# Optimization experiments

Hardware: AMD Instinct MI355X
Metric: run time of the kernel (lower is better)

The kernel has to match this reference:

```python
import jax, jax.numpy as jnp
import numpy as np

N_NODES = 100000
N_EDGES = 1600000
IN_FEATS = 128
HIDDEN = 128
NUM_CLASSES = 4


def setup_inputs() -> dict:
    key = jax.random.key(0)
    ks = jax.random.split(key, 8)
    features = jax.random.normal(ks[0], (N_NODES, IN_FEATS), dtype=jnp.float32)
    src = jax.random.randint(ks[1], (N_EDGES,), 0, N_NODES, dtype=jnp.int64)
    dst = jax.random.randint(ks[2], (N_EDGES,), 0, N_NODES, dtype=jnp.int64)
    s = 1.0 / np.sqrt(IN_FEATS)
    W1 = jax.random.normal(ks[3], (IN_FEATS, HIDDEN), dtype=jnp.float32) * s
    b1 = jnp.zeros((HIDDEN,), dtype=jnp.float32)
    W2 = jax.random.normal(ks[4], (HIDDEN, HIDDEN), dtype=jnp.float32) * s
    b2 = jnp.zeros((HIDDEN,), dtype=jnp.float32)
    Wc = jax.random.normal(ks[5], (HIDDEN, NUM_CLASSES), dtype=jnp.float32) * s
    bc = jnp.zeros((NUM_CLASSES,), dtype=jnp.float32)
    return {"features": features, "src": src, "dst": dst,
            "W1": W1, "b1": b1, "W2": W2, "b2": b2, "Wc": Wc, "bc": bc}


def _graph_conv(x, W, b, src, dst, n_nodes, activation=True):
    # DGL GraphConv, norm='both': D_out^{-1/2} A^T D_in... i.e. symmetric norm.
    ones = jnp.ones((src.shape[0],), dtype=x.dtype)
    deg_out = jnp.clip(jax.ops.segment_sum(ones, src, num_segments=n_nodes), 1.0)
    deg_in = jnp.clip(jax.ops.segment_sum(ones, dst, num_segments=n_nodes), 1.0)
    # scale sources, project (in >= out so matmul first, math-equivalent), gather-scatter
    h = (x * (deg_out ** -0.5)[:, None]) @ W            # [N, out]
    msg = h[src]                                         # [E, out] gather
    agg = jax.ops.segment_sum(msg, dst, num_segments=n_nodes)  # [N, out] scatter-add
    h = agg * (deg_in ** -0.5)[:, None] + b
    return jax.nn.relu(h) if activation else h


def reference(features, src, dst, W1, b1, W2, b2, Wc, bc):
    # eval-mode forward: dropout is identity
    n = features.shape[0]
    h = _graph_conv(features, W1, b1, src, dst, n, activation=True)
    h = _graph_conv(h, W2, b2, src, dst, n, activation=True)
    return h @ Wc + bc  # [N, num_classes] logits
```

## Files before the change

kernel.cpp:

```cpp
#include <hip/hip_runtime.h>
#include <hip/hip_fp16.h>
#include <math.h>

#define N_NODES 100000
#define N_EDGES 1600000
#define F 128
#define NBUK 196
#define BSH 9
#define BSZ 512
#define CAP 10240
#define NPART 784

typedef _Float16 half8 __attribute__((ext_vector_type(8)));
typedef float    f32x4 __attribute__((ext_vector_type(4)));
typedef int      i32x4 __attribute__((ext_vector_type(4)));

__global__ __launch_bounds__(256) void init_pack(int* __restrict__ curD,
                                                 int* __restrict__ curS,
                                                 _Float16* __restrict__ padrow1,
                                                 _Float16* __restrict__ padrow2,
                                                 const float* __restrict__ W1,
                                                 const float* __restrict__ W2,
                                                 _Float16* __restrict__ hi1,
                                                 _Float16* __restrict__ lo1,
                                                 _Float16* __restrict__ hi2,
                                                 _Float16* __restrict__ lo2)
{
    int t = threadIdx.x;
    if (blockIdx.x == 0) {
        if (t < NBUK) { curD[t] = t * CAP; curS[t] = t * CAP; }
        if (t < 16) reinterpret_cast<int4*>(padrow1)[t] = make_int4(0, 0, 0, 0);
        else if (t >= 32 && t < 48) reinterpret_cast<int4*>(padrow2)[t - 32] = make_int4(0, 0, 0, 0);
        return;
    }
    int gidx = (blockIdx.x - 1) * 256 + t;
    const float* W = (gidx < 16384) ? W1 : W2;
    _Float16* hi = (gidx < 16384) ? hi1 : hi2;
    _Float16* lo = (gidx < 16384) ? lo1 : lo2;
    int idx = gidx & 16383;
    int f = idx >> 9, r = idx & 511;
    int l = r >> 3, j = r & 7;
    int kc = f >> 3, ct = f & 7;
    int k = kc * 32 + (l >> 4) * 8 + j;
    int n = ct * 16 + (l & 15);
    float w = W[k * 128 + n];
    _Float16 h = (_Float16)w;
    hi[idx] = h;
    lo[idx] = (_Float16)(w - (float)h);
}

__global__ __launch_bounds__(512) void part_edges(const int* __restrict__ src,
                                                  const int* __restrict__ dst,
                                                  int* __restrict__ curD,
                                                  int* __restrict__ curS,
                                                  int* __restrict__ bukD,
                                                  unsigned short* __restrict__ bukS)
{
    __shared__ int hd[NBUK], hs[NBUK], bd[NBUK], bs[NBUK], cd[NBUK], cs[NBUK];
    const int tid = threadIdx.x;
    const int chunk = (((N_EDGES + NPART - 1) / NPART) + 3) & ~3;
    const int beg = blockIdx.x * chunk;
    const int end = min(beg + chunk, N_EDGES);
    if (beg >= end) return;
    if (tid < NBUK) { hd[tid] = 0; hs[tid] = 0; cd[tid] = 0; cs[tid] = 0; }
    __syncthreads();
    const int b4 = beg >> 2, e4 = end >> 2;
    const int i0 = b4 + tid;
    const bool v0 = i0 < e4;
    i32x4 d0 = {}, s0 = {};
    if (v0) {
        d0 = reinterpret_cast<const i32x4*>(dst)[i0];
        s0 = reinterpret_cast<const i32x4*>(src)[i0];
        atomicAdd(&hd[d0.x >> BSH], 1); atomicAdd(&hd[d0.y >> BSH], 1);
        atomicAdd(&hd[d0.z >> BSH], 1); atomicAdd(&hd[d0.w >> BSH], 1);
        atomicAdd(&hs[s0.x >> BSH], 1); atomicAdd(&hs[s0.y >> BSH], 1);
        atomicAdd(&hs[s0.z >> BSH], 1); atomicAdd(&hs[s0.w >> BSH], 1);
    }
    __syncthreads();
    if (tid < NBUK) {
        bd[tid] = hd[tid] ? atomicAdd(&curD[tid], hd[tid]) : 0;
        bs[tid] = hs[tid] ? atomicAdd(&curS[tid], hs[tid]) : 0;
    }
    __syncthreads();
    if (v0) {
        int dd[4] = { d0.x, d0.y, d0.z, d0.w };
        int ss[4] = { s0.x, s0.y, s0.z, s0.w };
        #pragma unroll
        for (int j = 0; j < 4; j++) {
            int bin = dd[j] >> BSH;
            int r = atomicAdd(&cd[bin], 1);
            bukD[bd[bin] + r] = ((dd[j] & 511) << 17) | ss[j];
            int bin2 = ss[j] >> BSH;
            int r2 = atomicAdd(&cs[bin2], 1);
            bukS[bs[bin2] + r2] = (unsigned short)(ss[j] & 511);
        }
    }
}

__global__ __launch_bounds__(512) void deg_out(const unsigned short* __restrict__ bukS,
                                               const int* __restrict__ curS,
                                               float* __restrict__ sout)
{
    __shared__ int h[BSZ];
    const int tid = threadIdx.x;
    const int n0 = blockIdx.x << BSH;
    const int lo = blockIdx.x * CAP, hi = curS[blockIdx.x];
    const int cnt = hi - lo;
    h[tid] = 0;
    __syncthreads();
    const uint4* p8 = reinterpret_cast<const uint4*>(bukS + lo);
    const int nv = cnt >> 3;
    for (int j = tid; j < nv; j += 512) {
        uint4 v = p8[j];
        atomicAdd(&h[v.x & 0xFFFF], 1); atomicAdd(&h[v.x >> 16], 1);
        atomicAdd(&h[v.y & 0xFFFF], 1); atomicAdd(&h[v.y >> 16], 1);
        atomicAdd(&h[v.z & 0xFFFF], 1); atomicAdd(&h[v.z >> 16], 1);
        atomicAdd(&h[v.w & 0xFFFF], 1); atomicAdd(&h[v.w >> 16], 1);
    }
    for (int i = lo + (nv << 3) + tid; i < hi; i += 512)
        atomicAdd(&h[bukS[i]], 1);
    __syncthreads();
    int node = n0 + tid;
    if (node < N_NODES) sout[node] = rsqrtf((float)max(h[tid], 1));
}

__global__ __launch_bounds__(512) void csr_gemm1(const int* __restrict__ bukD,
                                                 const int* __restrict__ curD,
                                                 int* __restrict__ row_ptr,
                                                 float* __restrict__ sin_,
                                                 int* __restrict__ col,
                                                 const float* __restrict__ X,
                                                 const _Float16* __restrict__ Whi,
                                                 const _Float16* __restrict__ Wlo,
                                                 const float* __restrict__ sout,
                                                 _Float16* __restrict__ Y, int N)
{
    __shared__ int h[BSZ], sc[BSZ], cur[BSZ];
    const int tid = threadIdx.x;

    if (blockIdx.x < NBUK) {
        const int n0 = blockIdx.x << BSH;
        const int lo = blockIdx.x * CAP, hi = curD[blockIdx.x];
        const int cnt = hi - lo;
        h[tid] = 0;
        __syncthreads();
        const i32x4* p4 = reinterpret_cast<const i32x4*>(bukD + lo);
        const int nv = cnt >> 2;
        for (int j = tid; j < nv; j += 512) {
            i32x4 v = p4[j];
            atomicAdd(&h[((unsigned)v.x) >> 17], 1);
            atomicAdd(&h[((unsigned)v.y) >> 17], 1);
            atomicAdd(&h[((unsigned)v.z) >> 17], 1);
            atomicAdd(&h[((unsigned)v.w) >> 17], 1);
        }
        for (int i = lo + (nv << 2) + tid; i < hi; i += 512)
            atomicAdd(&h[((unsigned)bukD[i]) >> 17], 1);
        __syncthreads();
        int own = h[tid];
        int own4 = (own + 3) & ~3;
        sc[tid] = own4;
        __syncthreads();
        for (int off = 1; off < 512; off <<= 1) {
            int u = (tid >= off) ? sc[tid - off] : 0;
            __syncthreads();
            sc[tid] += u;
            __syncthreads();
        }
        int ex = sc[tid] - own4;
        cur[tid] = ex;
        int node = n0 + tid;
        if (node < N_NODES) {
            row_ptr[2 * node]     = lo + ex;
            row_ptr[2 * node + 1] = lo + ex + own4;
            sin_[node] = rsqrtf((float)max(own, 1));
        }
        __syncthreads();
        for (int j = tid; j < nv; j += 512) {
            i32x4 v = p4[j];
            int pv[4] = { v.x, v.y, v.z, v.w };
            #pragma unroll
            for (int q = 0; q < 4; q++) {
                int p = pv[q];
                int r = atomicAdd(&cur[((unsigned)p) >> 17], 1);
                col[lo + r] = p & 0x1FFFF;
            }
        }
        for (int i = lo + (nv << 2) + tid; i < hi; i += 512) {
            int p = bukD[i];
            int r = atomicAdd(&cur[((unsigned)p) >> 17], 1);
            col[lo + r] = p & 0x1FFFF;
        }
        for (int k = own; k < own4; k++)
            col[lo + ex + k] = N_NODES;
        return;
    }

    const int l = tid & 63, w = tid >> 6;
    const int quad = l >> 4, m = l & 15;
    const int row0 = (blockIdx.x - NBUK) * 256;
    const half8* Bh = reinterpret_cast<const half8*>(Whi);
    const half8* Bl = reinterpret_cast<const half8*>(Wlo);

    f32x4 acc[2][8] = {};

    for (int kc = 0; kc < 4; kc++) {
        half8 ah[2];
        #pragma unroll
        for (int rt = 0; rt < 2; rt++) {
            int grow = row0 + w * 32 + rt * 16 + m;
            float4 xa = make_float4(0.f, 0.f, 0.f, 0.f), xb = xa;
            if (grow < N) {
                const float4* Xp = reinterpret_cast<const float4*>(X) + (size_t)grow * 32 + kc * 8 + quad * 2;
                xa = Xp[0]; xb = Xp[1];
            }
            ah[rt][0] = (_Float16)xa.x; ah[rt][1] = (_Float16)xa.y;
            ah[rt][2] = (_Float16)xa.z; ah[rt][3] = (_Float16)xa.w;
            ah[rt][4] = (_Float16)xb.x; ah[rt][5] = (_Float16)xb.y;
            ah[rt][6] = (_Float16)xb.z; ah[rt][7] = (_Float16)xb.w;
        }
        #pragma unroll
        for (int ct = 0; ct < 8; ct++) {
            int f = kc * 8 + ct;
            half8 bh = Bh[f * 64 + l];
            half8 bl = Bl[f * 64 + l];
            #pragma unroll
            for (int rt = 0; rt < 2; rt++) {
                acc[rt][ct] = __builtin_amdgcn_mfma_f32_16x16x32_f16(ah[rt], bh, acc[rt][ct], 0, 0, 0);
                acc[rt][ct] = __builtin_amdgcn_mfma_f32_16x16x32_f16(ah[rt], bl, acc[rt][ct], 0, 0, 0);
            }
        }
    }

    #pragma unroll
    for (int rt = 0; rt < 2; rt++) {
        #pragma unroll
        for (int r = 0; r < 4; r++) {
            int grow = row0 + w * 32 + rt * 16 + quad * 4 + r;
            if (grow < N) {
                float s = sout[grow];
                #pragma unroll
                for (int ct = 0; ct < 8; ct++)
                    Y[(size_t)grow * 128 + ct * 16 + m] = (_Float16)(acc[rt][ct][r] * s);
            }
        }
    }
}

#define ACCU(vv) \
    a0 += (float)vv[0]; a1 += (float)vv[1]; a2 += (float)vv[2]; a3 += (float)vv[3]; \
    a4 += (float)vv[4]; a5 += (float)vv[5]; a6 += (float)vv[6]; a7 += (float)vv[7];

__global__ __launch_bounds__(256) void gather_gemm2(const _Float16* __restrict__ Hh,
                                                    const int* __restrict__ row_ptr,
                                                    const int* __restrict__ col,
                                                    const float* __restrict__ sin_,
                                                    const float* __restrict__ bias,
                                                    const _Float16* __restrict__ Whi,
                                                    const _Float16* __restrict__ Wlo,
                                                    const float* __restrict__ sout,
                                                    _Float16* __restrict__ Y)
{
    __shared__ _Float16 At[16][128];
    const int tid = threadIdx.x;
    const int sub  = tid & 15;
    const int g0   = tid >> 4;
    const int node = blockIdx.x * 16 + g0;
    const int beg = row_ptr[2 * node], end = row_ptr[2 * node + 1];
    const half8* __restrict__ H8 = reinterpret_cast<const half8*>(Hh);

    float a0 = 0.f, a1 = 0.f, a2 = 0.f, a3 = 0.f, a4 = 0.f, a5 = 0.f, a6 = 0.f, a7 = 0.f;
    int i = beg;
    for (; i + 8 <= end; i += 8) {
        int4 ca = *reinterpret_cast<const int4*>(col + i);
        int4 cb = *reinterpret_cast<const int4*>(col + i + 4);
        half8 v0 = H8[((size_t)ca.x << 4) | sub];
        half8 v1 = H8[((size_t)ca.y << 4) | sub];
        half8 v2 = H8[((size_t)ca.z << 4) | sub];
        half8 v3 = H8[((size_t)ca.w << 4) | sub];
        half8 v4 = H8[((size_t)cb.x << 4) | sub];
        half8 v5 = H8[((size_t)cb.y << 4) | sub];
        half8 v6 = H8[((size_t)cb.z << 4) | sub];
        half8 v7 = H8[((size_t)cb.w << 4) | sub];
        ACCU(v0) ACCU(v1) ACCU(v2) ACCU(v3)
        ACCU(v4) ACCU(v5) ACCU(v6) ACCU(v7)
    }
    if (i < end) {
        int4 ca = *reinterpret_cast<const int4*>(col + i);
        half8 v0 = H8[((size_t)ca.x << 4) | sub];
        half8 v1 = H8[((size_t)ca.y << 4) | sub];
        half8 v2 = H8[((size_t)ca.z << 4) | sub];
        half8 v3 = H8[((size_t)ca.w << 4) | sub];
        ACCU(v0) ACCU(v1) ACCU(v2) ACCU(v3)
    }
    {
        float scn = sin_[node];
        const float4* B4 = reinterpret_cast<const float4*>(bias);
        float4 bA = B4[2 * sub], bB = B4[2 * sub + 1];
        half8 o;
        o[0] = (_Float16)fmaxf(fmaf(a0, scn, bA.x), 0.f);
        o[1] = (_Float16)fmaxf(fmaf(a1, scn, bA.y), 0.f);
        o[2] = (_Float16)fmaxf(fmaf(a2, scn, bA.z), 0.f);
        o[3] = (_Float16)fmaxf(fmaf(a3, scn, bA.w), 0.f);
        o[4] = (_Float16)fmaxf(fmaf(a4, scn, bB.x), 0.f);
        o[5] = (_Float16)fmaxf(fmaf(a5, scn, bB.y), 0.f);
        o[6] = (_Float16)fmaxf(fmaf(a6, scn, bB.z), 0.f);
        o[7] = (_Float16)fmaxf(fmaf(a7, scn, bB.w), 0.f);
        int wc = sub ^ (g0 & 7);
        *reinterpret_cast<half8*>(&At[g0][wc * 8]) = o;
    }
    __syncthreads();

    const int l = tid & 63, w = tid >> 6;
    const int quad = l >> 4, m = l & 15;
    const half8* Bh = reinterpret_cast<const half8*>(Whi);
    const half8* Bl = reinterpret_cast<const half8*>(Wlo);

    f32x4 acc0 = {}, acc1 = {};
    #pragma unroll
    for (int kc = 0; kc < 4; kc++) {
        int rc = (kc * 4 + quad) ^ (m & 7);
        half8 a = *reinterpret_cast<const half8*>(&At[m][rc * 8]);
        int f0 = kc * 8 + w * 2;
        half8 bh0 = Bh[f0 * 64 + l];
        half8 bl0 = Bl[f0 * 64 + l];
        half8 bh1 = Bh[(f0 + 1) * 64 + l];
        half8 bl1 = Bl[(f0 + 1) * 64 + l];
        acc0 = __builtin_amdgcn_mfma_f32_16x16x32_f16(a, bh0, acc0, 0, 0, 0);
        acc0 = __builtin_amdgcn_mfma_f32_16x16x32_f16(a, bl0, acc0, 0, 0, 0);
        acc1 = __builtin_amdgcn_mfma_f32_16x16x32_f16(a, bh1, acc1, 0, 0, 0);
        acc1 = __builtin_amdgcn_mfma_f32_16x16x32_f16(a, bl1, acc1, 0, 0, 0);
    }

    const int rbase = blockIdx.x * 16 + quad * 4;
    const int c0 = (w * 2) * 16 + m;
    #pragma unroll
    for (int r = 0; r < 4; r++) {
        int grow = rbase + r;
        float s = sout[grow];
        Y[(size_t)grow * 128 + c0]      = (_Float16)(acc0[r] * s);
        Y[(size_t)grow * 128 + c0 + 16] = (_Float16)(acc1[r] * s);
    }
}

__global__ __launch_bounds__(256) void gather_cls(const _Float16* __restrict__ Hh,
                                                  const int* __restrict__ row_ptr,
                                                  const int* __restrict__ col,
                                                  const float* __restrict__ sin_,
                                                  const float* __restrict__ bias,
                                                  const float* __restrict__ Wc,
                                                  const float* __restrict__ bc,
                                                  float* __restrict__ out, int N)
{
    __shared__ float4 Wcs[128];
    for (int t = threadIdx.x; t < 128; t += 256)
        Wcs[t] = reinterpret_cast<const float4*>(Wc)[t];
    __syncthreads();

    const int sub  = threadIdx.x & 15;
    const int node = blockIdx.x * 16 + (threadIdx.x >> 4);
    if (node >= N) return;
    const int beg = row_ptr[2 * node], end = row_ptr[2 * node + 1];
    const half8* __restrict__ H8 = reinterpret_cast<const half8*>(Hh);

    float a0 = 0.f, a1 = 0.f, a2 = 0.f, a3 = 0.f, a4 = 0.f, a5 = 0.f, a6 = 0.f, a7 = 0.f;
    int i = beg;
    for (; i + 8 <= end; i += 8) {
        int4 ca = *reinterpret_cast<const int4*>(col + i);
        int4 cb = *reinterpret_cast<const int4*>(col + i + 4);
        half8 v0 = H8[((size_t)ca.x << 4) | sub];
        half8 v1 = H8[((size_t)ca.y << 4) | sub];
        half8 v2 = H8[((size_t)ca.z << 4) | sub];
        half8 v3 = H8[((size_t)ca.w << 4) | sub];
        half8 v4 = H8[((size_t)cb.x << 4) | sub];
        half8 v5 = H8[((size_t)cb.y << 4) | sub];
        half8 v6 = H8[((size_t)cb.z << 4) | sub];
        half8 v7 = H8[((size_t)cb.w << 4) | sub];
        ACCU(v0) ACCU(v1) ACCU(v2) ACCU(v3)
        ACCU(v4) ACCU(v5) ACCU(v6) ACCU(v7)
    }
    if (i < end) {
        int4 ca = *reinterpret_cast<const int4*>(col + i);
        half8 v0 = H8[((size_t)ca.x << 4) | sub];
        half8 v1 = H8[((size_t)ca.y << 4) | sub];
        half8 v2 = H8[((size_t)ca.z << 4) | sub];
        half8 v3 = H8[((size_t)ca.w << 4) | sub];
        ACCU(v0) ACCU(v1) ACCU(v2) ACCU(v3)
    }
    float scn = sin_[node];
    const float4* B4 = reinterpret_cast<const float4*>(bias);
    float4 bA = B4[2 * sub], bB = B4[2 * sub + 1];
    float h0 = fmaxf(fmaf(a0, scn, bA.x), 0.f);
    float h1 = fmaxf(fmaf(a1, scn, bA.y), 0.f);
    float h2 = fmaxf(fmaf(a2, scn, bA.z), 0.f);
    float h3 = fmaxf(fmaf(a3, scn, bA.w), 0.f);
    float h4 = fmaxf(fmaf(a4, scn, bB.x), 0.f);
    float h5 = fmaxf(fmaf(a5, scn, bB.y), 0.f);
    float h6 = fmaxf(fmaf(a6, scn, bB.z), 0.f);
    float h7 = fmaxf(fmaf(a7, scn, bB.w), 0.f);

    float lx = 0.f, ly = 0.f, lz = 0.f, lw = 0.f;
    float4 w;
    w = Wcs[sub * 8 + 0]; lx = fmaf(h0, w.x, lx); ly = fmaf(h0, w.y, ly); lz = fmaf(h0, w.z, lz); lw = fmaf(h0, w.w, lw);
    w = Wcs[sub * 8 + 1]; lx = fmaf(h1, w.x, lx); ly = fmaf(h1, w.y, ly); lz = fmaf(h1, w.z, lz); lw = fmaf(h1, w.w, lw);
    w = Wcs[sub * 8 + 2]; lx = fmaf(h2, w.x, lx); ly = fmaf(h2, w.y, ly); lz = fmaf(h2, w.z, lz); lw = fmaf(h2, w.w, lw);
    w = Wcs[sub * 8 + 3]; lx = fmaf(h3, w.x, lx); ly = fmaf(h3, w.y, ly); lz = fmaf(h3, w.z, lz); lw = fmaf(h3, w.w, lw);
    w = Wcs[sub * 8 + 4]; lx = fmaf(h4, w.x, lx); ly = fmaf(h4, w.y, ly); lz = fmaf(h4, w.z, lz); lw = fmaf(h4, w.w, lw);
    w = Wcs[sub * 8 + 5]; lx = fmaf(h5, w.x, lx); ly = fmaf(h5, w.y, ly); lz = fmaf(h5, w.z, lz); lw = fmaf(h5, w.w, lw);
    w = Wcs[sub * 8 + 6]; lx = fmaf(h6, w.x, lx); ly = fmaf(h6, w.y, ly); lz = fmaf(h6, w.z, lz); lw = fmaf(h6, w.w, lw);
    w = Wcs[sub * 8 + 7]; lx = fmaf(h7, w.x, lx); ly = fmaf(h7, w.y, ly); lz = fmaf(h7, w.z, lz); lw = fmaf(h7, w.w, lw);

    #pragma unroll
    for (int m = 1; m < 16; m <<= 1) {
        lx += __shfl_xor(lx, m);
        ly += __shfl_xor(ly, m);
        lz += __shfl_xor(lz, m);
        lw += __shfl_xor(lw, m);
    }
    if (sub == 0) {
        float4 bcv = reinterpret_cast<const float4*>(bc)[0];
        float4 r;
        r.x = lx + bcv.x; r.y = ly + bcv.y; r.z = lz + bcv.z; r.w = lw + bcv.w;
        reinterpret_cast<float4*>(out)[node] = r;
    }
}

extern "C" void kernel_launch(void* const* d_in, const int* in_sizes, int n_in,
                              void* d_out, int out_size, void* d_ws, size_t ws_size,
                              hipStream_t stream)
{
    const float* features = (const float*)d_in[0];
    const int*   src      = (const int*)d_in[1];
    const int*   dst      = (const int*)d_in[2];
    const float* W1       = (const float*)d_in[3];
    const float* b1       = (const float*)d_in[4];
    const float* W2       = (const float*)d_in[5];
    const float* b2       = (const float*)d_in[6];
    const float* Wc       = (const float*)d_in[7];
    const float* bc       = (const float*)d_in[8];
    float* out = (float*)d_out;

    char* ws = (char*)d_ws;
    const size_t MB = 1 << 20;
    int* curD  = (int*)(ws + 0);
    int* curS  = (int*)(ws + 1024);
    _Float16* Whi1 = (_Float16*)(ws + 64 * 1024);
    _Float16* Wlo1 = (_Float16*)(ws + 96 * 1024);
    _Float16* Whi2 = (_Float16*)(ws + 128 * 1024);
    _Float16* Wlo2 = (_Float16*)(ws + 160 * 1024);
    float* sout    = (float*)(ws + 512 * 1024);
    float* sin_    = (float*)(ws + 1 * MB);
    int*   row_ptr = (int*)(ws + 2 * MB);
    int*   col     = (int*)(ws + 3 * MB);
    _Float16* hMsg = (_Float16*)(ws + 25 * MB);
    int*   bukD    = (int*)(ws + 52 * MB);
    unsigned short* bukS = (unsigned short*)(ws + 60 * MB);
    _Float16* hA   = (_Float16*)(ws + 52 * MB);

    const int N = N_NODES;
    const int NGB = (N + 15) / 16;

    init_pack<<<129, 256, 0, stream>>>(curD, curS,
                                       hMsg + (size_t)N * F, hA + (size_t)N * F,
                                       W1, W2, Whi1, Wlo1, Whi2, Wlo2);

    part_edges<<<NPART, 512, 0, stream>>>(src, dst, curD, curS, bukD, bukS);

    deg_out<<<NBUK, 512, 0, stream>>>(bukS, curS, sout);

    csr_gemm1<<<NBUK + 391, 512, 0, stream>>>(bukD, curD, row_ptr, sin_, col,
                                              features, Whi1, Wlo1, sout, hMsg, N);

    gather_gemm2<<<NGB, 256, 0, stream>>>(hMsg, row_ptr, col, sin_, b1,
                                          Whi2, Wlo2, sout, hA);

    gather_cls<<<NGB, 256, 0, stream>>>(hA, row_ptr, col, sin_, b2, Wc, bc, out, N);
}
```

Baseline: 285.1 us.

## Slice layer-2 features into column partitions for cache-local gather, split classifier

gather_gemm2 now writes its layer-2 message features as 8 column slices of 16 halves each, stored as separate planar arrays. A new gather_sl kernel runs the second-layer aggregation one slice per block, so each slice's working set (about 3.2 MB) can stay in cache while edges are gathered at random. It then writes ReLU'd fp16 hidden states, and a separate classifier kernel applies Wc. This adds an extra kernel launch and an fp16 round trip of the hidden state, and the column list is read eight times.

```diff
diff --git a/kernel.cpp b/kernel.cpp
--- a/kernel.cpp
+++ b/kernel.cpp
@@ -10,6 +10,8 @@
 #define BSZ 512
 #define CAP 10240
 #define NPART 784
+#define PST  1600016
+#define PS2  1600000
 
 typedef _Float16 half8 __attribute__((ext_vector_type(8)));
 typedef float    f32x4 __attribute__((ext_vector_type(4)));
@@ -18,7 +20,6 @@
 __global__ __launch_bounds__(256) void init_pack(int* __restrict__ curD,
                                                  int* __restrict__ curS,
                                                  _Float16* __restrict__ padrow1,
-                                                 _Float16* __restrict__ padrow2,
                                                  const float* __restrict__ W1,
                                                  const float* __restrict__ W2,
                                                  _Float16* __restrict__ hi1,
@@ -30,7 +31,6 @@
     if (blockIdx.x == 0) {
         if (t < NBUK) { curD[t] = t * CAP; curS[t] = t * CAP; }
         if (t < 16) reinterpret_cast<int4*>(padrow1)[t] = make_int4(0, 0, 0, 0);
-        else if (t >= 32 && t < 48) reinterpret_cast<int4*>(padrow2)[t - 32] = make_int4(0, 0, 0, 0);
         return;
     }
     int gidx = (blockIdx.x - 1) * 256 + t;
@@ -262,6 +262,11 @@
 {
     __shared__ _Float16 At[16][128];
     const int tid = threadIdx.x;
+    if (blockIdx.x == 0 && tid < 16) {
+        int p = tid >> 1, half = tid & 1;
+        _Float16* dst = Y + (size_t)p * PST + (size_t)N_NODES * 16 + half * 8;
+        *reinterpret_cast<int4*>(dst) = make_int4(0, 0, 0, 0);
+    }
     const int sub  = tid & 15;
     const int g0   = tid >> 4;
     const int node = blockIdx.x * 16 + g0;
@@ -332,96 +337,103 @@
     }
 
     const int rbase = blockIdx.x * 16 + quad * 4;
-    const int c0 = (w * 2) * 16 + m;
+    const size_t pb0 = (size_t)(w * 2) * PST;
+    const size_t pb1 = pb0 + PST;
     #pragma unroll
     for (int r = 0; r < 4; r++) {
         int grow = rbase + r;
         float s = sout[grow];
-        Y[(size_t)grow * 128 + c0]      = (_Float16)(acc0[r] * s);
-        Y[(size_t)grow * 128 + c0 + 16] = (_Float16)(acc1[r] * s);
-    }
-}
-
-__global__ __launch_bounds__(256) void gather_cls(const _Float16* __restrict__ Hh,
-                                                  const int* __restrict__ row_ptr,
-                                                  const int* __restrict__ col,
-                                                  const float* __restrict__ sin_,
-                                                  const float* __restrict__ bias,
-                                                  const float* __restrict__ Wc,
-                                                  const float* __restrict__ bc,
-                                                  float* __restrict__ out, int N)
-{
-    __shared__ float4 Wcs[128];
-    for (int t = threadIdx.x; t < 128; t += 256)
-        Wcs[t] = reinterpret_cast<const float4*>(Wc)[t];
-    __syncthreads();
-
-    const int sub  = threadIdx.x & 15;
-    const int node = blockIdx.x * 16 + (threadIdx.x >> 4);
+        Y[pb0 + (size_t)grow * 16 + m] = (_Float16)(acc0[r] * s);
+        Y[pb1 + (size_t)grow * 16 + m] = (_Float16)(acc1[r] * s);
+    }
+}
+
+__global__ __launch_bounds__(256) void gather_sl(const _Float16* __restrict__ Ha,
+                                                 const int* __restrict__ row_ptr,
+                                                 const int* __restrict__ col,
+                                                 const float* __restrict__ sin_,
+                                                 const float* __restrict__ bias,
+                                                 _Float16* __restrict__ Y2, int N)
+{
+    const int slice = blockIdx.x & 7;
+    const int g     = blockIdx.x >> 3;
+    const int j     = threadIdx.x & 1;
+    const int node  = g * 128 + (threadIdx.x >> 1);
     if (node >= N) return;
     const int beg = row_ptr[2 * node], end = row_ptr[2 * node + 1];
-    const half8* __restrict__ H8 = reinterpret_cast<const half8*>(Hh);
+    const half8* __restrict__ P = reinterpret_cast<const half8*>(Ha + (size_t)slice * PST);
 
     float a0 = 0.f, a1 = 0.f, a2 = 0.f, a3 = 0.f, a4 = 0.f, a5 = 0.f, a6 = 0.f, a7 = 0.f;
     int i = beg;
     for (; i + 8 <= end; i += 8) {
         int4 ca = *reinterpret_cast<const int4*>(col + i);
         int4 cb = *reinterpret_cast<const int4*>(col + i + 4);
-        half8 v0 = H8[((size_t)ca.x << 4) | sub];
-        half8 v1 = H8[((size_t)ca.y << 4) | sub];
-        half8 v2 = H8[((size_t)ca.z << 4) | sub];
-        half8 v3 = H8[((size_t)ca.w << 4) | sub];
-        half8 v4 = H8[((size_t)cb.x << 4) | sub];
-        half8 v5 = H8[((size_t)cb.y << 4) | sub];
-        half8 v6 = H8[((size_t)cb.z << 4) | sub];
-        half8 v7 = H8[((size_t)cb.w << 4) | sub];
+        half8 v0 = P[((size_t)ca.x << 1) | j];
+        half8 v1 = P[((size_t)ca.y << 1) | j];
+        half8 v2 = P[((size_t)ca.z << 1) | j];
+        half8 v3 = P[((size_t)ca.w << 1) | j];
+        half8 v4 = P[((size_t)cb.x << 1) | j];
+        half8 v5 = P[((size_t)cb.y << 1) | j];
+        half8 v6 = P[((size_t)cb.z << 1) | j];
+        half8 v7 = P[((size_t)cb.w << 1) | j];
         ACCU(v0) ACCU(v1) ACCU(v2) ACCU(v3)
         ACCU(v4) ACCU(v5) ACCU(v6) ACCU(v7)
     }
     if (i < end) {
         int4 ca = *reinterpret_cast<const int4*>(col + i);
-        half8 v0 = H8[((size_t)ca.x << 4) | sub];
-        half8 v1 = H8[((size_t)ca.y << 4) | sub];
-        half8 v2 = H8[((size_t)ca.z << 4) | sub];
-        half8 v3 = H8[((size_t)ca.w << 4) | sub];
+        half8 v0 = P[((size_t)ca.x << 1) | j];
+        half8 v1 = P[((size_t)ca.y << 1) | j];
+        half8 v2 = P[((size_t)ca.z << 1) | j];
+        half8 v3 = P[((size_t)ca.w << 1) | j];
         ACCU(v0) ACCU(v1) ACCU(v2) ACCU(v3)
     }
     float scn = sin_[node];
     const float4* B4 = reinterpret_cast<const float4*>(bias);
-    float4 bA = B4[2 * sub], bB = B4[2 * sub + 1];
-    float h0 = fmaxf(fmaf(a0, scn, bA.x), 0.f);
-    float h1 = fmaxf(fmaf(a1, scn, bA.y), 0.f);
-    float h2 = fmaxf(fmaf(a2, scn, bA.z), 0.f);
-    float h3 = fmaxf(fmaf(a3, scn, bA.w), 0.f);
-    float h4 = fmaxf(fmaf(a4, scn, bB.x), 0.f);
-    float h5 = fmaxf(fmaf(a5, scn, bB.y), 0.f);
-    float h6 = fmaxf(fmaf(a6, scn, bB.z), 0.f);
-    float h7 = fmaxf(fmaf(a7, scn, bB.w), 0.f);
-
-    float lx = 0.f, ly = 0.f, lz = 0.f, lw = 0.f;
-    float4 w;
-    w = Wcs[sub * 8 + 0]; lx = fmaf(h0, w.x, lx); ly = fmaf(h0, w.y, ly); lz = fmaf(h0, w.z, lz); lw = fmaf(h0, w.w, lw);
-    w = Wcs[sub * 8 + 1]; lx = fmaf(h1, w.x, lx); ly = fmaf(h1, w.y, ly); lz = fmaf(h1, w.z, lz); lw = fmaf(h1, w.w, lw);
-    w = Wcs[sub * 8 + 2]; lx = fmaf(h2, w.x, lx); ly = fmaf(h2, w.y, ly); lz = fmaf(h2, w.z, lz); lw = fmaf(h2, w.w, lw);
-    w = Wcs[sub * 8 + 3]; lx = fmaf(h3, w.x, lx); ly = fmaf(h3, w.y, ly); lz = fmaf(h3, w.z, lz); lw = fmaf(h3, w.w, lw);
-    w = Wcs[sub * 8 + 4]; lx = fmaf(h4, w.x, lx); ly = fmaf(h4, w.y, ly); lz = fmaf(h4, w.z, lz); lw = fmaf(h4, w.w, lw);
-    w = Wcs[sub * 8 + 5]; lx = fmaf(h5, w.x, lx); ly = fmaf(h5, w.y, ly); lz = fmaf(h5, w.z, lz); lw = fmaf(h5, w.w, lw);
-    w = Wcs[sub * 8 + 6]; lx = fmaf(h6, w.x, lx); ly = fmaf(h6, w.y, ly); lz = fmaf(h6, w.z, lz); lw = fmaf(h6, w.w, lw);
-    w = Wcs[sub * 8 + 7]; lx = fmaf(h7, w.x, lx); ly = fmaf(h7, w.y, ly); lz = fmaf(h7, w.z, lz); lw = fmaf(h7, w.w, lw);
-
+    float4 bA = B4[slice * 4 + j * 2], bB = B4[slice * 4 + j * 2 + 1];
+    half8 o;
+    o[0] = (_Float16)fmaxf(fmaf(a0, scn, bA.x), 0.f);
+    o[1] = (_Float16)fmaxf(fmaf(a1, scn, bA.y), 0.f);
+    o[2] = (_Float16)fmaxf(fmaf(a2, scn, bA.z), 0.f);
+    o[3] = (_Float16)fmaxf(fmaf(a3, scn, bA.w), 0.f);
+    o[4] = (_Float16)fmaxf(fmaf(a4, scn, bB.x), 0.f);
+    o[5] = (_Float16)fmaxf(fmaf(a5, scn, bB.y), 0.f);
+    o[6] = (_Float16)fmaxf(fmaf(a6, scn, bB.z), 0.f);
+    o[7] = (_Float16)fmaxf(fmaf(a7, scn, bB.w), 0.f);
+    reinterpret_cast<half8*>(Y2)[(size_t)slice * (PS2 / 8) + (size_t)node * 2 + j] = o;
+}
+
+__global__ __launch_bounds__(256) void classifier(const _Float16* __restrict__ H2,
+                                                  const float* __restrict__ Wc,
+                                                  const float* __restrict__ bc,
+                                                  float* __restrict__ out, int N)
+{
+    __shared__ float4 Wcs[128];
+    for (int t = threadIdx.x; t < 128; t += 256)
+        Wcs[t] = reinterpret_cast<const float4*>(Wc)[t];
+    __syncthreads();
+    int i = blockIdx.x * 256 + threadIdx.x;
+    if (i >= N) return;
+    float4 acc = reinterpret_cast<const float4*>(bc)[0];
     #pragma unroll
-    for (int m = 1; m < 16; m <<= 1) {
-        lx += __shfl_xor(lx, m);
-        ly += __shfl_xor(ly, m);
-        lz += __shfl_xor(lz, m);
-        lw += __shfl_xor(lw, m);
-    }
-    if (sub == 0) {
-        float4 bcv = reinterpret_cast<const float4*>(bc)[0];
-        float4 r;
-        r.x = lx + bcv.x; r.y = ly + bcv.y; r.z = lz + bcv.z; r.w = lw + bcv.w;
-        reinterpret_cast<float4*>(out)[node] = r;
-    }
+    for (int p = 0; p < 8; p++) {
+        const half8* hp = reinterpret_cast<const half8*>(H2 + (size_t)p * PS2 + (size_t)i * 16);
+        half8 x0 = hp[0], x1 = hp[1];
+        #pragma unroll
+        for (int k = 0; k < 8; k++) {
+            float f0 = (float)x0[k];
+            float4 w0 = Wcs[p * 16 + k];
+            acc.x = fmaf(f0, w0.x, acc.x); acc.y = fmaf(f0, w0.y, acc.y);
+            acc.z = fmaf(f0, w0.z, acc.z); acc.w = fmaf(f0, w0.w, acc.w);
+        }
+        #pragma unroll
+        for (int k = 0; k < 8; k++) {
+            float f1 = (float)x1[k];
+            float4 w1 = Wcs[p * 16 + 8 + k];
+            acc.x = fmaf(f1, w1.x, acc.x); acc.y = fmaf(f1, w1.y, acc.y);
+            acc.z = fmaf(f1, w1.z, acc.z); acc.w = fmaf(f1, w1.w, acc.w);
+        }
+    }
+    reinterpret_cast<float4*>(out)[i] = acc;
 }
 
 extern "C" void kernel_launch(void* const* d_in, const int* in_sizes, int n_in,
@@ -452,15 +464,16 @@
     int*   row_ptr = (int*)(ws + 2 * MB);
     int*   col     = (int*)(ws + 3 * MB);
     _Float16* hMsg = (_Float16*)(ws + 25 * MB);
+    _Float16* h2   = (_Float16*)(ws + 25 * MB);
     int*   bukD    = (int*)(ws + 52 * MB);
     unsigned short* bukS = (unsigned short*)(ws + 60 * MB);
     _Float16* hA   = (_Float16*)(ws + 52 * MB);
 
     const int N = N_NODES;
-    const int NGB = (N + 15) / 16;
-
-    init_pack<<<129, 256, 0, stream>>>(curD, curS,
-                                       hMsg + (size_t)N * F, hA + (size_t)N * F,
+    const int NGB  = (N + 15) / 16;
+    const int NGSL = ((N + 127) / 128) * 8;
+
+    init_pack<<<129, 256, 0, stream>>>(curD, curS, hMsg + (size_t)N * F,
                                        W1, W2, Whi1, Wlo1, Whi2, Wlo2);
 
     part_edges<<<NPART, 512, 0, stream>>>(src, dst, curD, curS, bukD, bukS);
@@ -473,5 +486,7 @@
     gather_gemm2<<<NGB, 256, 0, stream>>>(hMsg, row_ptr, col, sin_, b1,
                                           Whi2, Wlo2, sout, hA);
 
-    gather_cls<<<NGB, 256, 0, stream>>>(hA, row_ptr, col, sin_, b2, Wc, bc, out, N);
-}
+    gather_sl<<<NGSL, 256, 0, stream>>>(hA, row_ptr, col, sin_, b2, h2, N);
+
+    classifier<<<(N + 255) / 256, 256, 0, stream>>>(h2, Wc, bc, out, N);
+}
```

After: 314.0 us. 1.1x slower.
